# Performance work log

Measured on AMD Instinct MI355X. Metric: run time of the kernel, lower is better.

Reference implementation:

```python
import jax, jax.numpy as jnp
import numpy as np

N = 50000
E = 625000
D_IN = 128
D_OUT = 128
NEG_SLOPE = 0.01  # torch LeakyReLU default


def setup_inputs() -> dict:
    key = jax.random.key(0)
    k1, k2, k3, k4, k5, k6, k7, k8 = jax.random.split(key, 8)
    features = jax.random.normal(k1, (N, D_IN), dtype=jnp.float32)
    target = jax.random.randint(k2, (E,), 0, N, dtype=jnp.int64)
    neighbor = jax.random.randint(k3, (E,), 0, N, dtype=jnp.int64)
    values = jax.random.uniform(k4, (E,), dtype=jnp.float32)
    # nn.Linear params (kaiming-uniform-ish init: U(-1/sqrt(in), 1/sqrt(in)))
    bound = 1.0 / np.sqrt(D_IN)
    W1 = jax.random.uniform(k5, (D_OUT, D_IN), minval=-bound, maxval=bound, dtype=jnp.float32)
    b1 = jax.random.uniform(k6, (D_OUT,), minval=-bound, maxval=bound, dtype=jnp.float32)
    W2 = jax.random.uniform(k7, (D_OUT, D_IN), minval=-bound, maxval=bound, dtype=jnp.float32)
    b2 = jax.random.uniform(k8, (D_OUT,), minval=-bound, maxval=bound, dtype=jnp.float32)
    return {"features": features, "target": target, "neighbor": neighbor,
            "values": values, "W1": W1, "b1": b1, "W2": W2, "b2": b2}


def reference(features, target, neighbor, values, W1, b1, W2, b2):
    # gather-scale: msg[e] = features[neighbor[e]] * values[e]
    msg = features[neighbor] * values[:, None]              # (E, D_IN)
    # scatter-add into target nodes
    h_neigh = jax.ops.segment_sum(msg, target, num_segments=N)  # (N, D_IN)
    # dual linear fusion + leaky relu
    h = (features + h_neigh) @ W1.T + b1 + (features * h_neigh) @ W2.T + b2
    return jnp.where(h >= 0, h, NEG_SLOPE * h)
```

## Files before the change

kernel.cpp:

```cpp
#include <hip/hip_runtime.h>

#define D 128
#define CAP 32
#define EPT 8
#define NEG_SLOPE 0.01f

typedef float v4f __attribute__((ext_vector_type(4)));
typedef short short8 __attribute__((ext_vector_type(8)));

static __device__ __forceinline__ short f2bf(float f) {
    unsigned u = __float_as_uint(f);
    unsigned r = (u + 0x7fffu + ((u >> 16) & 1u)) >> 16;
    return (short)r;
}
static __device__ __forceinline__ float bflo(unsigned u) { return __uint_as_float(u << 16); }
static __device__ __forceinline__ float bfhi(unsigned u) { return __uint_as_float(u & 0xffff0000u); }
static __device__ __forceinline__ unsigned packbf(float x, float y) {
    return (unsigned)(unsigned short)f2bf(x) | ((unsigned)(unsigned short)f2bf(y) << 16);
}

__global__ __launch_bounds__(256) void convbucket_kernel(const float* __restrict__ feat,
                                                         const float* __restrict__ W1,
                                                         const float* __restrict__ W2,
                                                         const int* __restrict__ tgt,
                                                         const int* __restrict__ nbr,
                                                         const float* __restrict__ vals,
                                                         unsigned* __restrict__ featbf,
                                                         short* __restrict__ Wbf,
                                                         int* __restrict__ deg,
                                                         unsigned* __restrict__ edata,
                                                         int4* __restrict__ ovf,
                                                         int* __restrict__ ovf_cnt,
                                                         int nPairs, int E, int nbB) {
    if ((int)blockIdx.x < nbB) {
        int base = (blockIdx.x * 256 + threadIdx.x) * EPT;
#pragma unroll
        for (int k = 0; k < EPT; k++) {
            int e = base + k;
            if (e < E) {
                int t    = tgt[e];
                int slot = atomicAdd(&deg[t], 1);
                if (slot < CAP) {
                    unsigned ent = ((unsigned)nbr[e] << 16) |
                                   (unsigned)(unsigned short)f2bf(vals[e]);
                    edata[((unsigned)t << 5) + slot] = ent;
                } else {
                    int o = atomicAdd(ovf_cnt, 1);
                    int4 ov;
                    ov.x = t;
                    ov.y = nbr[e];
                    ov.z = __float_as_int(vals[e]);
                    ov.w = 0;
                    ovf[o] = ov;
                }
            }
        }
    } else {
        int i = (blockIdx.x - nbB) * 256 + threadIdx.x;
        if (i < nPairs) {
            float2 f = ((const float2*)feat)[i];
            featbf[i] = packbf(f.x, f.y);
        }
        if (i < D * D) {
            Wbf[i]         = f2bf(W1[i]);
            Wbf[D * D + i] = f2bf(W2[i]);
        }
    }
}

__global__ __launch_bounds__(256) void gather_kernel(const unsigned* __restrict__ featbf,
                                                     const unsigned* __restrict__ edata,
                                                     const int* __restrict__ deg,
                                                     const int4* __restrict__ ovf,
                                                     const int* __restrict__ ovf_cnt,
                                                     unsigned* __restrict__ X1,
                                                     unsigned* __restrict__ X2,
                                                     int nNodes) {
    int wid  = (blockIdx.x * 256 + threadIdx.x) >> 6;
    int lane = threadIdx.x & 63;
    if (wid >= nNodes) return;
    int d  = deg[wid];
    int dd = d < CAP ? d : CAP;

    unsigned uf = featbf[(long)wid * (D / 2) + lane];

    float ax0 = 0.f, ay0 = 0.f, ax1 = 0.f, ay1 = 0.f;
    float ax2 = 0.f, ay2 = 0.f, ax3 = 0.f, ay3 = 0.f;

    {
        const unsigned* ep = edata + ((unsigned)wid << 5);
        int dm1 = dd - 1;
        for (int j = 0; j < dd; j += 8) {
            unsigned p0 = ep[min(j + 0, dm1)];
            unsigned p1 = ep[min(j + 1, dm1)];
            unsigned p2 = ep[min(j + 2, dm1)];
            unsigned p3 = ep[min(j + 3, dm1)];
            unsigned p4 = ep[min(j + 4, dm1)];
            unsigned p5 = ep[min(j + 5, dm1)];
            unsigned p6 = ep[min(j + 6, dm1)];
            unsigned p7 = ep[min(j + 7, dm1)];
            unsigned u0 = featbf[(long)(p0 >> 16) * (D / 2) + lane];
            unsigned u1 = featbf[(long)(p1 >> 16) * (D / 2) + lane];
            unsigned u2 = featbf[(long)(p2 >> 16) * (D / 2) + lane];
            unsigned u3 = featbf[(long)(p3 >> 16) * (D / 2) + lane];
            unsigned u4 = featbf[(long)(p4 >> 16) * (D / 2) + lane];
            unsigned u5 = featbf[(long)(p5 >> 16) * (D / 2) + lane];
            unsigned u6 = featbf[(long)(p6 >> 16) * (D / 2) + lane];
            unsigned u7 = featbf[(long)(p7 >> 16) * (D / 2) + lane];
            float v0 = (j + 0 < dd) ? bflo(p0) : 0.0f;
            float v1 = (j + 1 < dd) ? bflo(p1) : 0.0f;
            float v2 = (j + 2 < dd) ? bflo(p2) : 0.0f;
            float v3 = (j + 3 < dd) ? bflo(p3) : 0.0f;
            float v4 = (j + 4 < dd) ? bflo(p4) : 0.0f;
            float v5 = (j + 5 < dd) ? bflo(p5) : 0.0f;
            float v6 = (j + 6 < dd) ? bflo(p6) : 0.0f;
            float v7 = (j + 7 < dd) ? bflo(p7) : 0.0f;
            ax0 += bflo(u0) * v0; ay0 += bfhi(u0) * v0;
            ax1 += bflo(u1) * v1; ay1 += bfhi(u1) * v1;
            ax2 += bflo(u2) * v2; ay2 += bfhi(u2) * v2;
            ax3 += bflo(u3) * v3; ay3 += bfhi(u3) * v3;
            ax0 += bflo(u4) * v4; ay0 += bfhi(u4) * v4;
            ax1 += bflo(u5) * v5; ay1 += bfhi(u5) * v5;
            ax2 += bflo(u6) * v6; ay2 += bfhi(u6) * v6;
            ax3 += bflo(u7) * v7; ay3 += bfhi(u7) * v7;
        }
    }

    if (d > CAP) {
        int cnt = *ovf_cnt;
        for (int basek = 0; basek < cnt; basek += 64) {
            int k = basek + lane;
            int t = (k < cnt) ? ovf[k].x : -1;
            unsigned long long m = __ballot(t == wid);
            while (m) {
                int b = __ffsll((long long)m) - 1;
                m &= m - 1;
                int4  ov = ovf[basek + b];
                float v  = __int_as_float(ov.z);
                unsigned u = featbf[(long)ov.y * (D / 2) + lane];
                ax0 += bflo(u) * v;
                ay0 += bfhi(u) * v;
            }
        }
    }

    float accx = (ax0 + ax1) + (ax2 + ax3);
    float accy = (ay0 + ay1) + (ay2 + ay3);
    float fx = bflo(uf), fy = bfhi(uf);
    X1[(long)wid * (D / 2) + lane] = packbf(fx + accx, fy + accy);
    X2[(long)wid * (D / 2) + lane] = packbf(fx * accx, fy * accy);
}

__global__ __launch_bounds__(512) void gemm_kernel(const short* __restrict__ X1s,
                                                   const short* __restrict__ X2s,
                                                   const short* __restrict__ Wbf,
                                                   const float* __restrict__ b1,
                                                   const float* __restrict__ b2,
                                                   float* __restrict__ out, int nNodes) {
    __shared__ __align__(16) short sW[2 * D * D];

    int tid = threadIdx.x;
    for (int c = tid; c < 4096; c += 512) {
        int r  = c >> 4;
        int cc = c & 15;
        int pp = cc ^ (r & 15);
        *(short8*)(&sW[r * D + pp * 8]) = *(const short8*)(Wbf + c * 8);
    }
    __syncthreads();

    int lane = tid & 63;
    int wid  = (blockIdx.x * 512 + tid) >> 6;
    int m0   = wid * 32;
    if (m0 >= nNodes) return;
    bool t2 = (m0 + 16) < nNodes;

    int mrow = lane & 15;
    int quad = lane >> 4;

    float bias[8];
#pragma unroll
    for (int ot = 0; ot < 8; ot++) {
        int o = ot * 16 + mrow;
        bias[ot] = b1[o] + b2[o];
    }

    const short* xa1 = X1s + (long)(m0 + mrow) * D + quad * 8;
    const short* xa2 = X2s + (long)(m0 + mrow) * D + quad * 8;
    const short* xb1 = xa1 + 16 * D;
    const short* xb2 = xa2 + 16 * D;

    v4f acc[2][8];
#pragma unroll
    for (int t = 0; t < 2; t++)
#pragma unroll
        for (int i = 0; i < 8; i++) acc[t][i] = (v4f)(0.0f);

#pragma unroll
    for (int s = 0; s < 4; s++) {
        short8 a1 = *(const short8*)(xa1 + s * 32);
        short8 a2 = *(const short8*)(xa2 + s * 32);
        short8 c1, c2;
        if (t2) {
            c1 = *(const short8*)(xb1 + s * 32);
            c2 = *(const short8*)(xb2 + s * 32);
        }
        int pp = (s * 4 + quad) ^ mrow;
#pragma unroll
        for (int ot = 0; ot < 8; ot++) {
            int row = ot * 16 + mrow;
            short8 w1 = *(const short8*)(&sW[row * D + pp * 8]);
            short8 w2 = *(const short8*)(&sW[D * D + row * D + pp * 8]);
            acc[0][ot] = __builtin_amdgcn_mfma_f32_16x16x32_bf16(a1, w1, acc[0][ot], 0, 0, 0);
            acc[0][ot] = __builtin_amdgcn_mfma_f32_16x16x32_bf16(a2, w2, acc[0][ot], 0, 0, 0);
            if (t2) {
                acc[1][ot] = __builtin_amdgcn_mfma_f32_16x16x32_bf16(c1, w1, acc[1][ot], 0, 0, 0);
                acc[1][ot] = __builtin_amdgcn_mfma_f32_16x16x32_bf16(c2, w2, acc[1][ot], 0, 0, 0);
            }
        }
    }

#pragma unroll
    for (int ot = 0; ot < 8; ot++) {
        int o = ot * 16 + mrow;
#pragma unroll
        for (int r = 0; r < 4; r++) {
            int   node = m0 + quad * 4 + r;
            float v    = acc[0][ot][r] + bias[ot];
            out[(long)node * D + o] = (v >= 0.0f) ? v : NEG_SLOPE * v;
            if (t2) {
                float w = acc[1][ot][r] + bias[ot];
                out[(long)(node + 16) * D + o] = (w >= 0.0f) ? w : NEG_SLOPE * w;
            }
        }
    }
}

extern "C" void kernel_launch(void* const* d_in, const int* in_sizes, int n_in,
                              void* d_out, int out_size, void* d_ws, size_t ws_size,
                              hipStream_t stream) {
    const float* feat = (const float*)d_in[0];
    const int*   tgt  = (const int*)d_in[1];
    const int*   nbr  = (const int*)d_in[2];
    const float* vals = (const float*)d_in[3];
    const float* W1   = (const float*)d_in[4];
    const float* b1   = (const float*)d_in[5];
    const float* W2   = (const float*)d_in[6];
    const float* b2   = (const float*)d_in[7];
    float*       out  = (float*)d_out;

    int E      = in_sizes[1];
    int nNodes = out_size / D;

    int*      deg     = (int*)d_ws;
    int*      ovf_cnt = deg + nNodes;
    int4*     ovf     = (int4*)(deg + nNodes + 4);
    unsigned* edata   = (unsigned*)(ovf + E);
    short*    Wbf     = (short*)(edata + (long)nNodes * CAP);
    unsigned* featbf  = (unsigned*)(Wbf + 2 * D * D);
    unsigned* X1      = featbf + (long)nNodes * (D / 2);
    unsigned* X2      = X1 + (long)nNodes * (D / 2);

    int nPairs = nNodes * (D / 2);
    int nbB    = (E + 256 * EPT - 1) / (256 * EPT);
    int nbC    = (nPairs + 255) / 256;

    hipMemsetAsync(deg, 0, (size_t)(nNodes + 4) * sizeof(int), stream);
    convbucket_kernel<<<nbB + nbC, 256, 0, stream>>>(feat, W1, W2, tgt, nbr, vals,
                                                     featbf, Wbf, deg, edata, ovf, ovf_cnt,
                                                     nPairs, E, nbB);
    gather_kernel<<<(nNodes * 64 + 255) / 256, 256, 0, stream>>>(featbf, edata, deg, ovf, ovf_cnt,
                                                                 X1, X2, nNodes);

    int nPairTiles = (nNodes + 31) / 32;
    int nBlocks    = (nPairTiles + 7) / 8;
    gemm_kernel<<<nBlocks, 512, 0, stream>>>((const short*)X1, (const short*)X2, Wbf, b1, b2, out, nNodes);
}
```

Baseline: 164.9 us.

## Fuse gather and dual-GEMM into one kernel staging activations in LDS

Merges the neighbor-gather kernel and the MFMA GEMM kernel. Each wave gathers 16 nodes sequentially, writes the bf16 X1/X2 rows into a swizzled LDS tile, then runs MFMA directly from LDS. The X1/X2 round trip through global memory and one launch go away. Weights are now read from global memory or cache instead of LDS, and each wave handles 16 nodes serially, which cuts gather parallelism and latency hiding. The feature conversion pass also switches to float4 loads.

New measurement: 191.2 us. 1.16x slower.

```diff
diff --git a/kernel.cpp b/kernel.cpp
--- a/kernel.cpp
+++ b/kernel.cpp
@@ -31,7 +31,7 @@
                                                          unsigned* __restrict__ edata,
                                                          int4* __restrict__ ovf,
                                                          int* __restrict__ ovf_cnt,
-                                                         int nPairs, int E, int nbB) {
+                                                         int nQuads, int E, int nbB) {
     if ((int)blockIdx.x < nbB) {
         int base = (blockIdx.x * 256 + threadIdx.x) * EPT;
 #pragma unroll
@@ -57,9 +57,12 @@
         }
     } else {
         int i = (blockIdx.x - nbB) * 256 + threadIdx.x;
-        if (i < nPairs) {
-            float2 f = ((const float2*)feat)[i];
-            featbf[i] = packbf(f.x, f.y);
+        if (i < nQuads) {
+            float4 f = ((const float4*)feat)[i];
+            uint2 p;
+            p.x = packbf(f.x, f.y);
+            p.y = packbf(f.z, f.w);
+            ((uint2*)featbf)[i] = p;
         }
         if (i < D * D) {
             Wbf[i]         = f2bf(W1[i]);
@@ -68,111 +71,24 @@
     }
 }
 
-__global__ __launch_bounds__(256) void gather_kernel(const unsigned* __restrict__ featbf,
-                                                     const unsigned* __restrict__ edata,
-                                                     const int* __restrict__ deg,
-                                                     const int4* __restrict__ ovf,
-                                                     const int* __restrict__ ovf_cnt,
-                                                     unsigned* __restrict__ X1,
-                                                     unsigned* __restrict__ X2,
-                                                     int nNodes) {
-    int wid  = (blockIdx.x * 256 + threadIdx.x) >> 6;
-    int lane = threadIdx.x & 63;
-    if (wid >= nNodes) return;
-    int d  = deg[wid];
-    int dd = d < CAP ? d : CAP;
-
-    unsigned uf = featbf[(long)wid * (D / 2) + lane];
-
-    float ax0 = 0.f, ay0 = 0.f, ax1 = 0.f, ay1 = 0.f;
-    float ax2 = 0.f, ay2 = 0.f, ax3 = 0.f, ay3 = 0.f;
-
-    {
-        const unsigned* ep = edata + ((unsigned)wid << 5);
-        int dm1 = dd - 1;
-        for (int j = 0; j < dd; j += 8) {
-            unsigned p0 = ep[min(j + 0, dm1)];
-            unsigned p1 = ep[min(j + 1, dm1)];
-            unsigned p2 = ep[min(j + 2, dm1)];
-            unsigned p3 = ep[min(j + 3, dm1)];
-            unsigned p4 = ep[min(j + 4, dm1)];
-            unsigned p5 = ep[min(j + 5, dm1)];
-            unsigned p6 = ep[min(j + 6, dm1)];
-            unsigned p7 = ep[min(j + 7, dm1)];
-            unsigned u0 = featbf[(long)(p0 >> 16) * (D / 2) + lane];
-            unsigned u1 = featbf[(long)(p1 >> 16) * (D / 2) + lane];
-            unsigned u2 = featbf[(long)(p2 >> 16) * (D / 2) + lane];
-            unsigned u3 = featbf[(long)(p3 >> 16) * (D / 2) + lane];
-            unsigned u4 = featbf[(long)(p4 >> 16) * (D / 2) + lane];
-            unsigned u5 = featbf[(long)(p5 >> 16) * (D / 2) + lane];
-            unsigned u6 = featbf[(long)(p6 >> 16) * (D / 2) + lane];
-            unsigned u7 = featbf[(long)(p7 >> 16) * (D / 2) + lane];
-            float v0 = (j + 0 < dd) ? bflo(p0) : 0.0f;
-            float v1 = (j + 1 < dd) ? bflo(p1) : 0.0f;
-            float v2 = (j + 2 < dd) ? bflo(p2) : 0.0f;
-            float v3 = (j + 3 < dd) ? bflo(p3) : 0.0f;
-            float v4 = (j + 4 < dd) ? bflo(p4) : 0.0f;
-            float v5 = (j + 5 < dd) ? bflo(p5) : 0.0f;
-            float v6 = (j + 6 < dd) ? bflo(p6) : 0.0f;
-            float v7 = (j + 7 < dd) ? bflo(p7) : 0.0f;
-            ax0 += bflo(u0) * v0; ay0 += bfhi(u0) * v0;
-            ax1 += bflo(u1) * v1; ay1 += bfhi(u1) * v1;
-            ax2 += bflo(u2) * v2; ay2 += bfhi(u2) * v2;
-            ax3 += bflo(u3) * v3; ay3 += bfhi(u3) * v3;
-            ax0 += bflo(u4) * v4; ay0 += bfhi(u4) * v4;
-            ax1 += bflo(u5) * v5; ay1 += bfhi(u5) * v5;
-            ax2 += bflo(u6) * v6; ay2 += bfhi(u6) * v6;
-            ax3 += bflo(u7) * v7; ay3 += bfhi(u7) * v7;
-        }
-    }
-
-    if (d > CAP) {
-        int cnt = *ovf_cnt;
-        for (int basek = 0; basek < cnt; basek += 64) {
-            int k = basek + lane;
-            int t = (k < cnt) ? ovf[k].x : -1;
-            unsigned long long m = __ballot(t == wid);
-            while (m) {
-                int b = __ffsll((long long)m) - 1;
-                m &= m - 1;
-                int4  ov = ovf[basek + b];
-                float v  = __int_as_float(ov.z);
-                unsigned u = featbf[(long)ov.y * (D / 2) + lane];
-                ax0 += bflo(u) * v;
-                ay0 += bfhi(u) * v;
-            }
-        }
-    }
-
-    float accx = (ax0 + ax1) + (ax2 + ax3);
-    float accy = (ay0 + ay1) + (ay2 + ay3);
-    float fx = bflo(uf), fy = bfhi(uf);
-    X1[(long)wid * (D / 2) + lane] = packbf(fx + accx, fy + accy);
-    X2[(long)wid * (D / 2) + lane] = packbf(fx * accx, fy * accy);
-}
-
-__global__ __launch_bounds__(512) void gemm_kernel(const short* __restrict__ X1s,
-                                                   const short* __restrict__ X2s,
-                                                   const short* __restrict__ Wbf,
-                                                   const float* __restrict__ b1,
-                                                   const float* __restrict__ b2,
-                                                   float* __restrict__ out, int nNodes) {
-    __shared__ __align__(16) short sW[2 * D * D];
-
-    int tid = threadIdx.x;
-    for (int c = tid; c < 4096; c += 512) {
-        int r  = c >> 4;
-        int cc = c & 15;
-        int pp = cc ^ (r & 15);
-        *(short8*)(&sW[r * D + pp * 8]) = *(const short8*)(Wbf + c * 8);
-    }
-    __syncthreads();
-
+__global__ __launch_bounds__(256) void gathergemm_kernel(const unsigned* __restrict__ featbf,
+                                                         const unsigned* __restrict__ edata,
+                                                         const int* __restrict__ deg,
+                                                         const int4* __restrict__ ovf,
+                                                         const int* __restrict__ ovf_cnt,
+                                                         const short* __restrict__ Wbf,
+                                                         const float* __restrict__ b1,
+                                                         const float* __restrict__ b2,
+                                                         float* __restrict__ out,
+                                                         int nNodes) {
+    __shared__ __align__(16) unsigned sX[4][2][1024];
+
+    int tid  = threadIdx.x;
     int lane = tid & 63;
-    int wid  = (blockIdx.x * 512 + tid) >> 6;
-    int m0   = wid * 32;
+    int w    = tid >> 6;
+    int tile = blockIdx.x * 4 + w;
+    int m0   = tile * 16;
     if (m0 >= nNodes) return;
-    bool t2 = (m0 + 16) < nNodes;
 
     int mrow = lane & 15;
     int quad = lane >> 4;
@@ -184,38 +100,101 @@
         bias[ot] = b1[o] + b2[o];
     }
 
-    const short* xa1 = X1s + (long)(m0 + mrow) * D + quad * 8;
-    const short* xa2 = X2s + (long)(m0 + mrow) * D + quad * 8;
-    const short* xb1 = xa1 + 16 * D;
-    const short* xb2 = xa2 + 16 * D;
-
-    v4f acc[2][8];
-#pragma unroll
-    for (int t = 0; t < 2; t++)
-#pragma unroll
-        for (int i = 0; i < 8; i++) acc[t][i] = (v4f)(0.0f);
+    int degv = deg[min(m0 + mrow, nNodes - 1)];
+
+    for (int n = 0; n < 16; n++) {
+        int node = m0 + n;
+        int d    = (node < nNodes) ? __shfl(degv, n) : 0;
+        int dd   = d < CAP ? d : CAP;
+
+        unsigned uf = featbf[(long)min(node, nNodes - 1) * (D / 2) + lane];
+
+        float ax0 = 0.f, ay0 = 0.f, ax1 = 0.f, ay1 = 0.f;
+        float ax2 = 0.f, ay2 = 0.f, ax3 = 0.f, ay3 = 0.f;
+
+        {
+            const unsigned* ep = edata + ((unsigned)node << 5);
+            int dm1 = dd - 1;
+            for (int j = 0; j < dd; j += 8) {
+                unsigned p0 = ep[min(j + 0, dm1)];
+                unsigned p1 = ep[min(j + 1, dm1)];
+                unsigned p2 = ep[min(j + 2, dm1)];
+                unsigned p3 = ep[min(j + 3, dm1)];
+                unsigned p4 = ep[min(j + 4, dm1)];
+                unsigned p5 = ep[min(j + 5, dm1)];
+                unsigned p6 = ep[min(j + 6, dm1)];
+                unsigned p7 = ep[min(j + 7, dm1)];
+                unsigned u0 = featbf[(long)(p0 >> 16) * (D / 2) + lane];
+                unsigned u1 = featbf[(long)(p1 >> 16) * (D / 2) + lane];
+                unsigned u2 = featbf[(long)(p2 >> 16) * (D / 2) + lane];
+                unsigned u3 = featbf[(long)(p3 >> 16) * (D / 2) + lane];
+                unsigned u4 = featbf[(long)(p4 >> 16) * (D / 2) + lane];
+                unsigned u5 = featbf[(long)(p5 >> 16) * (D / 2) + lane];
+                unsigned u6 = featbf[(long)(p6 >> 16) * (D / 2) + lane];
+                unsigned u7 = featbf[(long)(p7 >> 16) * (D / 2) + lane];
+                float v0 = (j + 0 < dd) ? bflo(p0) : 0.0f;
+                float v1 = (j + 1 < dd) ? bflo(p1) : 0.0f;
+                float v2 = (j + 2 < dd) ? bflo(p2) : 0.0f;
+                float v3 = (j + 3 < dd) ? bflo(p3) : 0.0f;
+                float v4 = (j + 4 < dd) ? bflo(p4) : 0.0f;
+                float v5 = (j + 5 < dd) ? bflo(p5) : 0.0f;
+                float v6 = (j + 6 < dd) ? bflo(p6) : 0.0f;
+                float v7 = (j + 7 < dd) ? bflo(p7) : 0.0f;
+                ax0 += bflo(u0) * v0; ay0 += bfhi(u0) * v0;
+                ax1 += bflo(u1) * v1; ay1 += bfhi(u1) * v1;
+                ax2 += bflo(u2) * v2; ay2 += bfhi(u2) * v2;
+                ax3 += bflo(u3) * v3; ay3 += bfhi(u3) * v3;
+                ax0 += bflo(u4) * v4; ay0 += bfhi(u4) * v4;
+                ax1 += bflo(u5) * v5; ay1 += bfhi(u5) * v5;
+                ax2 += bflo(u6) * v6; ay2 += bfhi(u6) * v6;
+                ax3 += bflo(u7) * v7; ay3 += bfhi(u7) * v7;
+            }
+        }
+
+        if (d > CAP) {
+            int cnt = *ovf_cnt;
+            for (int basek = 0; basek < cnt; basek += 64) {
+                int k = basek + lane;
+                int t = (k < cnt) ? ovf[k].x : -1;
+                unsigned long long m = __ballot(t == node);
+                while (m) {
+                    int b = __ffsll((long long)m) - 1;
+                    m &= m - 1;
+                    int4  ov = ovf[basek + b];
+                    float v  = __int_as_float(ov.z);
+                    unsigned u = featbf[(long)ov.y * (D / 2) + lane];
+                    ax0 += bflo(u) * v;
+                    ay0 += bfhi(u) * v;
+                }
+            }
+        }
+
+        float accx = (ax0 + ax1) + (ax2 + ax3);
+        float accy = (ay0 + ay1) + (ay2 + ay3);
+        float fx = bflo(uf), fy = bfhi(uf);
+        int idx = n * 64 + (((lane >> 2) ^ n) << 2) + (lane & 3);
+        sX[w][0][idx] = packbf(fx + accx, fy + accy);
+        sX[w][1][idx] = packbf(fx * accx, fy * accy);
+    }
+
+    v4f acc[8];
+#pragma unroll
+    for (int ot = 0; ot < 8; ot++) acc[ot] = (v4f)(0.0f);
 
 #pragma unroll
     for (int s = 0; s < 4; s++) {
-        short8 a1 = *(const short8*)(xa1 + s * 32);
-        short8 a2 = *(const short8*)(xa2 + s * 32);
-        short8 c1, c2;
-        if (t2) {
-            c1 = *(const short8*)(xb1 + s * 32);
-            c2 = *(const short8*)(xb2 + s * 32);
-        }
-        int pp = (s * 4 + quad) ^ mrow;
+        int ck = s * 4 + quad;
+        int pp = ck ^ mrow;
+        short8 a1 = *(const short8*)(&sX[w][0][mrow * 64 + pp * 4]);
+        short8 a2 = *(const short8*)(&sX[w][1][mrow * 64 + pp * 4]);
+        const short* wp = Wbf + ck * 8;
 #pragma unroll
         for (int ot = 0; ot < 8; ot++) {
             int row = ot * 16 + mrow;
-            short8 w1 = *(const short8*)(&sW[row * D + pp * 8]);
-            short8 w2 = *(const short8*)(&sW[D * D + row * D + pp * 8]);
-            acc[0][ot] = __builtin_amdgcn_mfma_f32_16x16x32_bf16(a1, w1, acc[0][ot], 0, 0, 0);
-            acc[0][ot] = __builtin_amdgcn_mfma_f32_16x16x32_bf16(a2, w2, acc[0][ot], 0, 0, 0);
-            if (t2) {
-                acc[1][ot] = __builtin_amdgcn_mfma_f32_16x16x32_bf16(c1, w1, acc[1][ot], 0, 0, 0);
-                acc[1][ot] = __builtin_amdgcn_mfma_f32_16x16x32_bf16(c2, w2, acc[1][ot], 0, 0, 0);
-            }
+            short8 w1 = *(const short8*)(wp + row * D);
+            short8 w2 = *(const short8*)(wp + D * D + row * D);
+            acc[ot] = __builtin_amdgcn_mfma_f32_16x16x32_bf16(a1, w1, acc[ot], 0, 0, 0);
+            acc[ot] = __builtin_amdgcn_mfma_f32_16x16x32_bf16(a2, w2, acc[ot], 0, 0, 0);
         }
     }
 
@@ -224,12 +203,10 @@
         int o = ot * 16 + mrow;
 #pragma unroll
         for (int r = 0; r < 4; r++) {
-            int   node = m0 + quad * 4 + r;
-            float v    = acc[0][ot][r] + bias[ot];
-            out[(long)node * D + o] = (v >= 0.0f) ? v : NEG_SLOPE * v;
-            if (t2) {
-                float w = acc[1][ot][r] + bias[ot];
-                out[(long)(node + 16) * D + o] = (w >= 0.0f) ? w : NEG_SLOPE * w;
+            int node = m0 + quad * 4 + r;
+            if (node < nNodes) {
+                float v = acc[ot][r] + bias[ot];
+                out[(long)node * D + o] = (v >= 0.0f) ? v : NEG_SLOPE * v;
             }
         }
     }
@@ -257,21 +234,18 @@
     unsigned* edata   = (unsigned*)(ovf + E);
     short*    Wbf     = (short*)(edata + (long)nNodes * CAP);
     unsigned* featbf  = (unsigned*)(Wbf + 2 * D * D);
-    unsigned* X1      = featbf + (long)nNodes * (D / 2);
-    unsigned* X2      = X1 + (long)nNodes * (D / 2);
-
-    int nPairs = nNodes * (D / 2);
+
+    int nQuads = nNodes * (D / 4);
     int nbB    = (E + 256 * EPT - 1) / (256 * EPT);
-    int nbC    = (nPairs + 255) / 256;
+    int nbC    = (nQuads + 255) / 256;
 
     hipMemsetAsync(deg, 0, (size_t)(nNodes + 4) * sizeof(int), stream);
     convbucket_kernel<<<nbB + nbC, 256, 0, stream>>>(feat, W1, W2, tgt, nbr, vals,
                                                      featbf, Wbf, deg, edata, ovf, ovf_cnt,
-                                                     nPairs, E, nbB);
-    gather_kernel<<<(nNodes * 64 + 255) / 256, 256, 0, stream>>>(featbf, edata, deg, ovf, ovf_cnt,
-                                                                 X1, X2, nNodes);
-
-    int nPairTiles = (nNodes + 31) / 32;
-    int nBlocks    = (nPairTiles + 7) / 8;
-    gemm_kernel<<<nBlocks, 512, 0, stream>>>((const short*)X1, (const short*)X2, Wbf, b1, b2, out, nNodes);
-}
+                                                     nQuads, E, nbB);
+
+    int nTiles  = (nNodes + 15) / 16;
+    int nBlocks = (nTiles + 3) / 4;
+    gathergemm_kernel<<<nBlocks, 256, 0, stream>>>(featbf, edata, deg, ovf, ovf_cnt,
+                                                   Wbf, b1, b2, out, nNodes);
+}
```
